# Optimization experiments

Hardware: AMD Instinct MI355X
Metric: run time of the kernel (lower is better)

Reference implementation:

```python
import jax, jax.numpy as jnp
import numpy as np

NUM_STEPS = 3
NUM_HEADS = 8
HEAD_DIM = 128
EPS = 1e-5


def layernorm(x, g, b):
    mu = jnp.mean(x, -1, keepdims=True)
    var = jnp.mean(jnp.square(x - mu), -1, keepdims=True)
    return (x - mu) * jax.lax.rsqrt(var + EPS) * g + b


def entmax15(x):
    # Exact entmax-1.5 along last axis (Peters & Martins 2019, sort-based).
    x = (x - jnp.max(x, -1, keepdims=True)) / 2.0
    xs = jnp.flip(jnp.sort(x, -1), -1)  # descending sort
    rho = jnp.arange(1, x.shape[-1] + 1, dtype=x.dtype)
    mean = jnp.cumsum(xs, -1) / rho
    meansq = jnp.cumsum(xs * xs, -1) / rho
    ss = rho * (meansq - jnp.square(mean))
    tau = mean - jnp.sqrt(jnp.clip((1.0 - ss) / rho, 0.0, None))
    support = jnp.sum(tau <= xs, -1, keepdims=True)
    tau_star = jnp.take_along_axis(tau, support - 1, -1)
    return jnp.square(jnp.clip(x - tau_star, 0.0, None))


def setup_inputs() -> dict:
    key = jax.random.key(0)
    ks = jax.random.split(key, 6)
    B, S, Hd, Md, N = 2, 1024, 2048, 1024, 2048
    THD = NUM_HEADS * HEAD_DIM
    return {
        "hidden": jax.random.normal(ks[0], (B, S, Hd), jnp.float32),
        "memory": jax.random.normal(ks[1], (N, Md), jnp.float32),
        "Wq": jax.random.normal(ks[2], (THD, Hd), jnp.float32) / np.float32(np.sqrt(Hd)),
        "Wk": jax.random.normal(ks[3], (THD, Md), jnp.float32) / np.float32(np.sqrt(Md)),
        "Wv": jax.random.normal(ks[4], (THD, Md), jnp.float32) / np.float32(np.sqrt(Md)),
        "Wo": jax.random.normal(ks[5], (Hd, THD), jnp.float32) / np.float32(np.sqrt(THD)),
        "log_beta": jnp.full((NUM_HEADS,), float(np.log(1.0 / np.sqrt(HEAD_DIM))), jnp.float32),
        "g_state": jnp.ones((Hd,), jnp.float32),
        "b_state": jnp.zeros((Hd,), jnp.float32),
        "g_mem": jnp.ones((Md,), jnp.float32),
        "b_mem": jnp.zeros((Md,), jnp.float32),
    }


def reference(hidden, memory, Wq, Wk, Wv, Wo, log_beta, g_state, b_state, g_mem, b_mem):
    B, S, _ = hidden.shape
    N = memory.shape[0]
    H, hd = NUM_HEADS, HEAD_DIM
    # projections
    Q = layernorm(hidden, g_state, b_state) @ Wq.T            # (B,S,H*hd)
    mn = layernorm(memory, g_mem, b_mem)                      # (N,Md)
    K = (mn @ Wk.T).reshape(N, H, hd).transpose(1, 0, 2)      # (H,N,hd)
    V = (mn @ Wv.T).reshape(N, H, hd).transpose(1, 0, 2)      # (H,N,hd)
    xi = Q.reshape(B, S, H, hd).transpose(0, 2, 1, 3)          # (B,H,S,hd)
    beta = jnp.exp(log_beta)[None, :, None, None]
    for _ in range(NUM_STEPS):
        scores = jnp.einsum('bhsd,hnd->bhsn', xi, K) * beta    # (B,H,S,N)
        w = entmax15(scores)
        xi = jnp.einsum('bhsn,hnd->bhsd', w, V)
    out = xi.transpose(0, 2, 1, 3).reshape(B, S, H * hd) @ Wo.T  # (B,S,hidden_dim)
    return out
```

## Files before the change

kernel.cpp:

```cpp
#include <hip/hip_runtime.h>

typedef _Float16 half8 __attribute__((ext_vector_type(8)));
typedef _Float16 hv4 __attribute__((ext_vector_type(4)));
typedef _Float16 h2 __attribute__((ext_vector_type(2)));
typedef float fv4 __attribute__((ext_vector_type(4)));

typedef __attribute__((address_space(3))) unsigned lds_u32;
typedef const __attribute__((address_space(1))) unsigned glb_u32;

#if defined(__has_builtin)
#if __has_builtin(__builtin_amdgcn_fdot2)
#define FDOT2(a, b, c) __builtin_amdgcn_fdot2((a), (b), (c), false)
#endif
#endif
#ifndef FDOT2
#define FDOT2(a, b, c) ((c) + (float)(a)[0] * (float)(b)[0] + (float)(a)[1] * (float)(b)[1])
#endif

__device__ __forceinline__ h2 pkrtz(float a, float b) {
  return __builtin_bit_cast(h2, __builtin_amdgcn_cvt_pkrtz(a, b));
}

__device__ __forceinline__ void gll16(const void* g, void* l) {
  __builtin_amdgcn_global_load_lds((glb_u32*)g, (lds_u32*)l, 16, 0, 0);
}

__device__ __forceinline__ void ln_body(const float* __restrict__ in, const float* __restrict__ g,
                                        const float* __restrict__ bb, _Float16* __restrict__ out,
                                        int ncols, int row) {
  __shared__ float sm[8];
  int t = threadIdx.x;
  const float* rp = in + (size_t)row * ncols;
  int nv = ncols >> 10;
  fv4 v[2];
  float s1 = 0.f, s2 = 0.f;
#pragma unroll
  for (int c = 0; c < 2; ++c)
    if (c < nv) {
      v[c] = *(const fv4*)(rp + c * 1024 + t * 4);
#pragma unroll
      for (int j = 0; j < 4; ++j) { s1 += v[c][j]; s2 += v[c][j] * v[c][j]; }
    }
#pragma unroll
  for (int off = 32; off > 0; off >>= 1) { s1 += __shfl_xor(s1, off, 64); s2 += __shfl_xor(s2, off, 64); }
  int w = t >> 6;
  if ((t & 63) == 0) { sm[w] = s1; sm[4 + w] = s2; }
  __syncthreads();
  s1 = sm[0] + sm[1] + sm[2] + sm[3];
  s2 = sm[4] + sm[5] + sm[6] + sm[7];
  float inv = 1.0f / (float)ncols;
  float mu = s1 * inv;
  float var = s2 * inv - mu * mu;
  float rstd = rsqrtf(var + 1e-5f);
#pragma unroll
  for (int c = 0; c < 2; ++c)
    if (c < nv) {
      int col = c * 1024 + t * 4;
      fv4 gg = *(const fv4*)(g + col);
      fv4 bv = *(const fv4*)(bb + col);
      hv4 o;
#pragma unroll
      for (int j = 0; j < 4; ++j) o[j] = (_Float16)(((v[c][j] - mu) * rstd) * gg[j] + bv[j]);
      *(hv4*)(out + (size_t)row * ncols + col) = o;
    }
}

__global__ __launch_bounds__(256) void ln_all(const float* __restrict__ hid,
                                              const float* __restrict__ mem,
                                              const float* __restrict__ gs, const float* __restrict__ bs,
                                              const float* __restrict__ gm, const float* __restrict__ bm,
                                              _Float16* __restrict__ oh, _Float16* __restrict__ om) {
  int b = blockIdx.x;
  if (b < 2048) ln_body(hid, gs, bs, oh, 2048, b);
  else ln_body(mem, gm, bm, om, 1024, b - 2048);
}

__global__ __launch_bounds__(256) void cast_all(const float* __restrict__ s0, _Float16* __restrict__ d0,
                                                const float* __restrict__ s1, _Float16* __restrict__ d1,
                                                const float* __restrict__ s2, _Float16* __restrict__ d2,
                                                const float* __restrict__ s3, _Float16* __restrict__ d3) {
  int b = blockIdx.x;
  const float* s;
  _Float16* d;
  int off;
  if (b < 2048) { s = s0; d = d0; off = b; }
  else if (b < 3072) { s = s1; d = d1; off = b - 2048; }
  else if (b < 4096) { s = s2; d = d2; off = b - 3072; }
  else { s = s3; d = d3; off = b - 4096; }
  int i = (off * 256 + threadIdx.x) << 2;
  fv4 f = *(const fv4*)(s + i);
  hv4 h;
#pragma unroll
  for (int j = 0; j < 4; ++j) h[j] = (_Float16)f[j];
  *(hv4*)(d + i) = h;
}

__global__ __launch_bounds__(256) void reduce_split(const float* __restrict__ parts, int ns,
                                                    long long stride,
                                                    _Float16* __restrict__ hi, int n) {
  int i = (blockIdx.x * 256 + threadIdx.x) << 2;
  if (i < n) {
    fv4 s = *(const fv4*)(parts + i);
    for (int j = 1; j < ns; ++j) {
      fv4 v = *(const fv4*)(parts + (size_t)j * stride + i);
      s += v;
    }
    hv4 h;
#pragma unroll
    for (int j = 0; j < 4; ++j) h[j] = (_Float16)s[j];
    *(hv4*)(hi + i) = h;
  }
}

__global__ __launch_bounds__(256, 3) void fused_step(const _Float16* __restrict__ xi,
                                                     const _Float16* __restrict__ kp,
                                                     const _Float16* __restrict__ vt,
                                                     const float* __restrict__ log_beta,
                                                     _Float16* __restrict__ xo) {
  __shared__ __align__(16) _Float16 ring[4 * 3 * 2048];
  __shared__ float red[384];
  float* red4 = (float*)ring;

  int t = threadIdx.x;
  int wv = t >> 6, l = t & 63;
  int lr = l & 15, quad = l >> 4;

  int id = blockIdx.x;
  int h = id & 7;
  int rbb = id >> 3;
  int b = rbb >> 6;
  int r0 = (rbb & 63) << 4;

  const _Float16* xiP = xi + ((size_t)(b * 1024 + r0)) * 1024 + h * 128;
  const _Float16* kP = kp + (size_t)h * 128;
  const _Float16* vP = vt + (size_t)h * 128 * 2048;
  int sbase = wv * 512;

  _Float16* ringW = &ring[wv * 6144];

  float a05 = 0.5f * __expf(log_beta[h]);

  half8 bx[4];
#pragma unroll
  for (int c = 0; c < 4; ++c)
    bx[c] = *(const half8*)(xiP + (size_t)lr * 1024 + c * 32 + quad * 8);
  asm volatile("s_waitcnt vmcnt(0)" ::: "memory");

  int srl = l >> 2;
  int scs = ((l & 3) ^ ((l >> 3) & 3)) << 3;
  int rsw = (lr >> 1) & 3;
  int vsh = ((l & 1) ^ ((l >> 3) & 1)) * 8;
  int hsr = ((quad >> 1) ^ ((lr >> 2) & 1));

  auto stageK = [&](int f) {
    const _Float16* src = kP + (size_t)(sbase + f * 16 + srl) * 1024 + scs;
    _Float16* dst = ringW + (f % 3) * 2048;
#pragma unroll
    for (int g = 0; g < 4; ++g) gll16(src + g * 32, dst + g * 512);
  };
  auto stageV = [&](int f) {
    const _Float16* src = vP + (size_t)(l >> 1) * 2048 + sbase + f * 16 + vsh;
    _Float16* dst = ringW + (f % 3) * 2048;
#pragma unroll
    for (int g = 0; g < 4; ++g) gll16(src + (size_t)g * 32 * 2048, dst + g * 512);
  };

  h2 pk[64];
  float msc = -3.0e38f;
  stageK(0); stageK(1);
#pragma unroll
  for (int f = 0; f < 32; ++f) {
    if (f < 31) asm volatile("s_waitcnt vmcnt(4)" ::: "memory");
    else asm volatile("s_waitcnt vmcnt(0)" ::: "memory");
    __builtin_amdgcn_sched_barrier(0);
    const _Float16* kb = ringW + (f % 3) * 2048;
    half8 ka[4];
#pragma unroll
    for (int g = 0; g < 4; ++g)
      ka[g] = *(const half8*)(kb + g * 512 + lr * 32 + ((quad ^ rsw) << 3));
    if (f + 2 < 32) stageK(f + 2);
    fv4 a = {0.f, 0.f, 0.f, 0.f};
    __builtin_amdgcn_s_setprio(1);
#pragma unroll
    for (int g = 0; g < 4; ++g)
      a = __builtin_amdgcn_mfma_f32_16x16x32_f16(ka[g], bx[g], a, 0, 0, 0);
    __builtin_amdgcn_s_setprio(0);
    msc = fmaxf(fmaxf(msc, fmaxf(a[0], a[1])), fmaxf(a[2], a[3]));
    pk[2 * f] = pkrtz(a05 * a[0], a05 * a[1]);
    pk[2 * f + 1] = pkrtz(a05 * a[2], a05 * a[3]);
  }

  msc = fmaxf(msc, __shfl_xor(msc, 16, 64));
  msc = fmaxf(msc, __shfl_xor(msc, 32, 64));
  if (l < 16) red[wv * 48 + l] = msc;
  __syncthreads();
  msc = fmaxf(fmaxf(red[lr], red[48 + lr]), fmaxf(red[96 + lr], red[144 + lr]));
  float xm = a05 * msc;
  h2 mpk = {(_Float16)xm, (_Float16)xm};
#pragma unroll
  for (int p = 0; p < 64; ++p) pk[p] = pk[p] - mpk;

  h2 one2 = {(_Float16)1.0f, (_Float16)1.0f};
  float tau = -1.0f;
  int par = 1;
#pragma unroll 1
  for (int it = 0; it < 14; ++it) {
    h2 tp = {(_Float16)tau, (_Float16)tau};
    float tq = (float)tp[0];
    float M1 = 0.f, M2 = 0.f;
    unsigned kc = 0;
#pragma unroll
    for (int p = 0; p < 64; ++p) {
      h2 y = __builtin_elementwise_max(pk[p], tp);
      M1 = FDOT2(y, one2, M1);
      M2 = FDOT2(y, y, M2);
      h2 d = tp - y;
      unsigned u = __builtin_bit_cast(unsigned, d);
      kc += (u >> 15) & 0x10001u;
    }
    float kf = (float)((kc & 0xffffu) + (kc >> 16));
    kf += __shfl_xor(kf, 16, 64); kf += __shfl_xor(kf, 32, 64);
    M1 += __shfl_xor(M1, 16, 64); M1 += __shfl_xor(M1, 32, 64);
    M2 += __shfl_xor(M2, 16, 64); M2 += __shfl_xor(M2, 32, 64);
    float* wr = red + par * 192 + wv * 48;
    if (l < 16) { wr[l] = kf; wr[16 + l] = M1; wr[32 + l] = M2; }
    __syncthreads();
    float C = 0.f, S1 = 0.f, S2 = 0.f;
#pragma unroll
    for (int w2 = 0; w2 < 4; ++w2) {
      const float* rr = red + par * 192 + w2 * 48;
      C += rr[lr]; S1 += rr[16 + lr]; S2 += rr[32 + lr];
    }
    par ^= 1;
    S1 = S1 - (2048.0f - C) * tq;
    S2 = S2 - (2048.0f - C) * tq * tq;
    float mean = S1 / C;
    float ssv = S2 - S1 * mean;
    float nt = mean - sqrtf(fmaxf((1.0f - ssv) / C, 0.0f));
    bool conv = fabsf(nt - tau) < 1e-4f;
    tau = nt;
    if (__all(conv)) break;
  }

  {
    h2 tp = {(_Float16)tau, (_Float16)tau};
#pragma unroll
    for (int p = 0; p < 64; ++p) {
      h2 y = __builtin_elementwise_max(pk[p], tp);
      h2 d = y - tp;
      pk[p] = d * d;
    }
  }

  fv4 acc[8] = {};
  stageV(0); stageV(1);
#pragma unroll
  for (int f = 0; f < 32; ++f) {
    if (f < 31) asm volatile("s_waitcnt vmcnt(4)" ::: "memory");
    else asm volatile("s_waitcnt vmcnt(0)" ::: "memory");
    __builtin_amdgcn_sched_barrier(0);
    const _Float16* vb = ringW + (f % 3) * 2048;
    hv4 bv[8];
#pragma unroll
    for (int ni = 0; ni < 8; ++ni)
      bv[ni] = *(const hv4*)(vb + (ni >> 1) * 512 + ((ni & 1) * 16 + lr) * 16 + hsr * 8 + (quad & 1) * 4);
    if (f + 2 < 32) stageV(f + 2);
    hv4 aw4 = {pk[2 * f][0], pk[2 * f][1], pk[2 * f + 1][0], pk[2 * f + 1][1]};
    __builtin_amdgcn_s_setprio(1);
#pragma unroll
    for (int ni = 0; ni < 8; ++ni)
      acc[ni] = __builtin_amdgcn_mfma_f32_16x16x16f16(aw4, bv[ni], acc[ni], 0, 0, 0);
    __builtin_amdgcn_s_setprio(0);
  }

  __syncthreads();
#pragma unroll
  for (int ni = 0; ni < 8; ++ni)
#pragma unroll
    for (int r = 0; r < 4; ++r)
      red4[wv * 2048 + (quad * 4 + r) * 128 + ni * 16 + lr] = acc[ni][r];
  __syncthreads();
#pragma unroll
  for (int g = 0; g < 2; ++g) {
    int idx = wv * 512 + g * 256 + l * 4;
    fv4 s = *(const fv4*)&red4[idx];
    s += *(const fv4*)&red4[idx + 2048];
    s += *(const fv4*)&red4[idx + 4096];
    s += *(const fv4*)&red4[idx + 6144];
    int row = idx >> 7, dim = idx & 127;
    hv4 o;
#pragma unroll
    for (int j = 0; j < 4; ++j) o[j] = (_Float16)s[j];
    *(hv4*)(xo + ((size_t)(b * 1024 + r0 + row)) * 1024 + h * 128 + dim) = o;
  }
}

struct GemmParams {
  const _Float16 *A, *B, *B2;
  _Float16 *C16, *C16b;
  float* C32;
  int K, lda, ldb;
  long long aSB, aSH, bSH;
  long long cSB, cSH, cOsR, cOsC;
  long long cOsRb, cOsCb;
  long long partStride;
  int outMode, outModeB, nsplit, dual;
  int gx, gy, swz;
};

__device__ __forceinline__ void gemm_body(const GemmParams& p, int bx, int by, int bz) {
  __shared__ __align__(16) _Float16 As[3][128 * 32];
  __shared__ __align__(16) _Float16 Bs[3][128 * 32];
  int t = threadIdx.x;
  int m0 = by * 128;
  int n0, kbeg, kend, ks = 0;
  if (p.nsplit > 1) {
    ks = bx % p.nsplit;
    n0 = (bx / p.nsplit) * 128;
    int kl = p.K / p.nsplit;
    kbeg = ks * kl;
    kend = kbeg + kl;
  } else {
    n0 = bx * 128;
    kbeg = 0;
    kend = p.K;
  }
  int bidx, h, job = 0;
  if (p.dual) { job = bz; bidx = 0; h = 0; }
  else { bidx = bz >> 3; h = bz & 7; }
  const _Float16* pA = p.A + bidx * p.aSB + h * p.aSH;
  const _Float16* pB = (job ? p.B2 : p.B) + h * p.bSH;

  fv4 acc[4][4] = {};
  int wv = t >> 6, l = t & 63, quad = l >> 4, lr = l & 15;
  int wm = (wv >> 1) * 64, wn = (wv & 1) * 64;
  int rl = l >> 2;
  int cs = (((l & 3) ^ ((l >> 3) & 3)) << 3);
  int rsw = (lr >> 1) & 3;

  auto STAGE = [&](int buf, int k0) {
#pragma unroll
    for (int v = 0; v < 2; ++v) {
      int rb = wv * 16 + v * 64;
      int r = rb + rl;
      gll16(pA + (size_t)(m0 + r) * p.lda + k0 + cs, &As[buf][rb * 32]);
      gll16(pB + (size_t)(n0 + r) * p.ldb + k0 + cs, &Bs[buf][rb * 32]);
    }
  };

  int nk = (kend - kbeg) >> 5;
  STAGE(0, kbeg);
  if (nk > 1) STAGE(1, kbeg + 32);
  int cur = 0;
  for (int ti = 0; ti < nk; ++ti) {
    if (ti + 1 < nk) asm volatile("s_waitcnt vmcnt(4)" ::: "memory");
    else asm volatile("s_waitcnt vmcnt(0)" ::: "memory");
    __builtin_amdgcn_s_barrier();
    __builtin_amdgcn_sched_barrier(0);
    if (ti + 2 < nk) {
      int nb = cur + 2;
      if (nb >= 3) nb -= 3;
      STAGE(nb, kbeg + ((ti + 2) << 5));
    }
    __builtin_amdgcn_sched_barrier(0);
    half8 ah[4], bh[4];
#pragma unroll
    for (int mi = 0; mi < 4; ++mi)
      ah[mi] = *(const half8*)&As[cur][(wm + mi * 16 + lr) * 32 + ((quad ^ rsw) << 3)];
#pragma unroll
    for (int ni = 0; ni < 4; ++ni)
      bh[ni] = *(const half8*)&Bs[cur][(wn + ni * 16 + lr) * 32 + ((quad ^ rsw) << 3)];
    __builtin_amdgcn_s_setprio(1);
#pragma unroll
    for (int mi = 0; mi < 4; ++mi)
#pragma unroll
      for (int ni = 0; ni < 4; ++ni)
        acc[mi][ni] = __builtin_amdgcn_mfma_f32_16x16x32_f16(ah[mi], bh[ni], acc[mi][ni], 0, 0, 0);
    __builtin_amdgcn_s_setprio(0);
    cur = (cur == 2) ? 0 : cur + 1;
  }

  int om = (p.dual && job) ? p.outModeB : p.outMode;
  _Float16* c16 = (p.dual && job) ? p.C16b : p.C16;
  long long osR = (p.dual && job) ? p.cOsRb : p.cOsR;
  long long osC = (p.dual && job) ? p.cOsCb : p.cOsC;
  float* c32 = p.C32 + (p.nsplit > 1 ? (long long)ks * p.partStride : 0);
  long long cOff = (long long)bidx * p.cSB + (long long)h * p.cSH;
#pragma unroll
  for (int mi = 0; mi < 4; ++mi)
#pragma unroll
    for (int ni = 0; ni < 4; ++ni) {
      int row = m0 + wm + mi * 16 + quad * 4;
      int col = n0 + wn + ni * 16 + lr;
#pragma unroll
      for (int r = 0; r < 4; ++r) {
        float val = acc[mi][ni][r];
        long long idx = cOff + (long long)(row + r) * osR + (long long)col * osC;
        if (om == 1) c32[idx] = val;
        else c16[idx] = (_Float16)val;
      }
    }
}

__global__ __launch_bounds__(256) void gemm_nt(GemmParams p) {
  int id = blockIdx.x;
  if (p.swz) {
    int q = (int)gridDim.x >> 3;
    id = (id & 7) * q + (id >> 3);
  }
  int bx = id % p.gx;
  int r = id / p.gx;
  gemm_body(p, bx, r % p.gy, r / p.gy);
}

__global__ __launch_bounds__(256) void gemm_pair(GemmParams a, GemmParams b, int na) {
  int id = blockIdx.x;
  if (id < na) {
    int bx = id % a.gx;
    int r = id / a.gx;
    gemm_body(a, bx, r % a.gy, r / a.gy);
  } else {
    int j = id - na;
    int bx = j % b.gx;
    int r = j / b.gx;
    gemm_body(b, bx, r % b.gy, r / b.gy);
  }
}

extern "C" void kernel_launch(void* const* d_in, const int* in_sizes, int n_in,
                              void* d_out, int out_size, void* d_ws, size_t ws_size,
                              hipStream_t stream) {
  const float* hidden = (const float*)d_in[0];
  const float* memory = (const float*)d_in[1];
  const float* Wq = (const float*)d_in[2];
  const float* Wk = (const float*)d_in[3];
  const float* Wv = (const float*)d_in[4];
  const float* Wo = (const float*)d_in[5];
  const float* log_beta = (const float*)d_in[6];
  const float* g_state = (const float*)d_in[7];
  const float* b_state = (const float*)d_in[8];
  const float* g_mem = (const float*)d_in[9];
  const float* b_mem = (const float*)d_in[10];

  char* w = (char*)d_ws;
  auto alloc = [&](size_t bytes) {
    char* r = w;
    w += (bytes + 255) & ~(size_t)255;
    return r;
  };
  _Float16* wq16 = (_Float16*)alloc(2097152 * 2);
  _Float16* wk16 = (_Float16*)alloc(1048576 * 2);
  _Float16* wv16 = (_Float16*)alloc(1048576 * 2);
  _Float16* wo16 = (_Float16*)alloc(2097152 * 2);
  _Float16* lnh16 = (_Float16*)alloc(4194304 * 2);
  _Float16* mn16 = (_Float16*)alloc(2097152 * 2);
  _Float16* kph = (_Float16*)alloc(2097152 * 2);
  _Float16* vt16 = (_Float16*)alloc(2097152 * 2);
  _Float16* xih = (_Float16*)alloc(2097152 * 2);
  float* parts = (float*)alloc((size_t)2 * 2097152 * 4);

  ln_all<<<4096, 256, 0, stream>>>(hidden, memory, g_state, b_state, g_mem, b_mem, lnh16, mn16);
  cast_all<<<6144, 256, 0, stream>>>(Wq, wq16, Wk, wk16, Wv, wv16, Wo, wo16);

  {
    GemmParams pq{};
    pq.A = lnh16; pq.lda = 2048;
    pq.B = wq16; pq.ldb = 2048;
    pq.K = 2048; pq.nsplit = 2;
    pq.C32 = parts; pq.outMode = 1; pq.partStride = 2097152;
    pq.cOsR = 1024; pq.cOsC = 1;
    pq.gx = 16; pq.gy = 16;

    GemmParams pkv{};
    pkv.A = mn16; pkv.lda = 1024;
    pkv.B = wk16; pkv.B2 = wv16; pkv.ldb = 1024;
    pkv.K = 1024; pkv.dual = 1;
    pkv.C16 = kph; pkv.outMode = 0; pkv.cOsR = 1024; pkv.cOsC = 1;
    pkv.C16b = vt16; pkv.outModeB = 0; pkv.cOsRb = 1; pkv.cOsCb = 2048;
    pkv.gx = 8; pkv.gy = 16;

    gemm_pair<<<512, 256, 0, stream>>>(pq, pkv, 256);
    reduce_split<<<2048, 256, 0, stream>>>(parts, 2, 2097152, xih, 2097152);
  }

  for (int step = 0; step < 3; ++step)
    fused_step<<<1024, 256, 0, stream>>>(xih, kph, vt16, log_beta, xih);

  {
    GemmParams p{};
    p.A = xih; p.lda = 1024;
    p.B = wo16; p.ldb = 1024;
    p.K = 1024;
    p.C32 = (float*)d_out; p.outMode = 1;
    p.cOsR = 2048; p.cOsC = 1;
    p.gx = 16; p.gy = 16; p.swz = 1;
    gemm_nt<<<256, 256, 0, stream>>>(p);
  }
}
```

Baseline: 489.4 us.

## Process 32 query rows per block in fused_step to reuse K/V tiles

Result: slower. 516.8 us (+5.6%).

```diff
diff --git a/kernel.cpp b/kernel.cpp
--- a/kernel.cpp
+++ b/kernel.cpp
@@ -23,6 +23,11 @@
 
 __device__ __forceinline__ void gll16(const void* g, void* l) {
   __builtin_amdgcn_global_load_lds((glb_u32*)g, (lds_u32*)l, 16, 0, 0);
+}
+
+__device__ __forceinline__ void barrier_lds() {
+  asm volatile("s_waitcnt lgkmcnt(0)" ::: "memory");
+  __builtin_amdgcn_s_barrier();
 }
 
 __device__ __forceinline__ void ln_body(const float* __restrict__ in, const float* __restrict__ g,
@@ -112,13 +117,13 @@
   }
 }
 
-__global__ __launch_bounds__(256, 3) void fused_step(const _Float16* __restrict__ xi,
+__global__ __launch_bounds__(256, 2) void fused_step(const _Float16* __restrict__ xi,
                                                      const _Float16* __restrict__ kp,
                                                      const _Float16* __restrict__ vt,
                                                      const float* __restrict__ log_beta,
                                                      _Float16* __restrict__ xo) {
   __shared__ __align__(16) _Float16 ring[4 * 3 * 2048];
-  __shared__ float red[384];
+  __shared__ float red[768];
   float* red4 = (float*)ring;
 
   int t = threadIdx.x;
@@ -128,8 +133,8 @@
   int id = blockIdx.x;
   int h = id & 7;
   int rbb = id >> 3;
-  int b = rbb >> 6;
-  int r0 = (rbb & 63) << 4;
+  int b = rbb >> 5;
+  int r0 = (rbb & 31) << 5;
 
   const _Float16* xiP = xi + ((size_t)(b * 1024 + r0)) * 1024 + h * 128;
   const _Float16* kP = kp + (size_t)h * 128;
@@ -140,10 +145,12 @@
 
   float a05 = 0.5f * __expf(log_beta[h]);
 
-  half8 bx[4];
-#pragma unroll
-  for (int c = 0; c < 4; ++c)
+  half8 bx[4], bx2[4];
+#pragma unroll
+  for (int c = 0; c < 4; ++c) {
     bx[c] = *(const half8*)(xiP + (size_t)lr * 1024 + c * 32 + quad * 8);
+    bx2[c] = *(const half8*)(xiP + (size_t)(16 + lr) * 1024 + c * 32 + quad * 8);
+  }
   asm volatile("s_waitcnt vmcnt(0)" ::: "memory");
 
   int srl = l >> 2;
@@ -165,8 +172,8 @@
     for (int g = 0; g < 4; ++g) gll16(src + (size_t)g * 32 * 2048, dst + g * 512);
   };
 
-  h2 pk[64];
-  float msc = -3.0e38f;
+  h2 pk[64], pk2[64];
+  float msc = -3.0e38f, msc2 = -3.0e38f;
   stageK(0); stageK(1);
 #pragma unroll
   for (int f = 0; f < 32; ++f) {
@@ -180,80 +187,113 @@
       ka[g] = *(const half8*)(kb + g * 512 + lr * 32 + ((quad ^ rsw) << 3));
     if (f + 2 < 32) stageK(f + 2);
     fv4 a = {0.f, 0.f, 0.f, 0.f};
+    fv4 a2 = {0.f, 0.f, 0.f, 0.f};
     __builtin_amdgcn_s_setprio(1);
 #pragma unroll
-    for (int g = 0; g < 4; ++g)
+    for (int g = 0; g < 4; ++g) {
       a = __builtin_amdgcn_mfma_f32_16x16x32_f16(ka[g], bx[g], a, 0, 0, 0);
+      a2 = __builtin_amdgcn_mfma_f32_16x16x32_f16(ka[g], bx2[g], a2, 0, 0, 0);
+    }
     __builtin_amdgcn_s_setprio(0);
     msc = fmaxf(fmaxf(msc, fmaxf(a[0], a[1])), fmaxf(a[2], a[3]));
+    msc2 = fmaxf(fmaxf(msc2, fmaxf(a2[0], a2[1])), fmaxf(a2[2], a2[3]));
     pk[2 * f] = pkrtz(a05 * a[0], a05 * a[1]);
     pk[2 * f + 1] = pkrtz(a05 * a[2], a05 * a[3]);
-  }
+    pk2[2 * f] = pkrtz(a05 * a2[0], a05 * a2[1]);
+    pk2[2 * f + 1] = pkrtz(a05 * a2[2], a05 * a2[3]);
+  }
+
+  asm volatile("s_waitcnt lgkmcnt(0)" ::: "memory");
+  __builtin_amdgcn_sched_barrier(0);
+  stageV(0); stageV(1);
 
   msc = fmaxf(msc, __shfl_xor(msc, 16, 64));
   msc = fmaxf(msc, __shfl_xor(msc, 32, 64));
-  if (l < 16) red[wv * 48 + l] = msc;
-  __syncthreads();
-  msc = fmaxf(fmaxf(red[lr], red[48 + lr]), fmaxf(red[96 + lr], red[144 + lr]));
-  float xm = a05 * msc;
-  h2 mpk = {(_Float16)xm, (_Float16)xm};
-#pragma unroll
-  for (int p = 0; p < 64; ++p) pk[p] = pk[p] - mpk;
+  msc2 = fmaxf(msc2, __shfl_xor(msc2, 16, 64));
+  msc2 = fmaxf(msc2, __shfl_xor(msc2, 32, 64));
+  if (l < 16) { red[wv * 16 + l] = msc; red[64 + wv * 16 + l] = msc2; }
+  barrier_lds();
+  float m = fmaxf(fmaxf(red[lr], red[16 + lr]), fmaxf(red[32 + lr], red[48 + lr]));
+  float m2 = fmaxf(fmaxf(red[64 + lr], red[80 + lr]), fmaxf(red[96 + lr], red[112 + lr]));
+  {
+    float xm = a05 * m, xm2 = a05 * m2;
+    h2 mpk = {(_Float16)xm, (_Float16)xm};
+    h2 mpk2 = {(_Float16)xm2, (_Float16)xm2};
+#pragma unroll
+    for (int p = 0; p < 64; ++p) { pk[p] = pk[p] - mpk; pk2[p] = pk2[p] - mpk2; }
+  }
 
   h2 one2 = {(_Float16)1.0f, (_Float16)1.0f};
-  float tau = -1.0f;
+  float tau = -1.0f, tau2 = -1.0f;
   int par = 1;
 #pragma unroll 1
   for (int it = 0; it < 14; ++it) {
     h2 tp = {(_Float16)tau, (_Float16)tau};
-    float tq = (float)tp[0];
-    float M1 = 0.f, M2 = 0.f;
-    unsigned kc = 0;
+    h2 tp2 = {(_Float16)tau2, (_Float16)tau2};
+    float tq = (float)tp[0], tq2 = (float)tp2[0];
+    float M1 = 0.f, M2 = 0.f, N1 = 0.f, N2 = 0.f;
+    unsigned kc = 0, kc2 = 0;
 #pragma unroll
     for (int p = 0; p < 64; ++p) {
       h2 y = __builtin_elementwise_max(pk[p], tp);
       M1 = FDOT2(y, one2, M1);
       M2 = FDOT2(y, y, M2);
-      h2 d = tp - y;
-      unsigned u = __builtin_bit_cast(unsigned, d);
+      unsigned u = __builtin_bit_cast(unsigned, h2(tp - y));
       kc += (u >> 15) & 0x10001u;
+      h2 y2 = __builtin_elementwise_max(pk2[p], tp2);
+      N1 = FDOT2(y2, one2, N1);
+      N2 = FDOT2(y2, y2, N2);
+      unsigned u2 = __builtin_bit_cast(unsigned, h2(tp2 - y2));
+      kc2 += (u2 >> 15) & 0x10001u;
     }
     float kf = (float)((kc & 0xffffu) + (kc >> 16));
+    float kf2 = (float)((kc2 & 0xffffu) + (kc2 >> 16));
     kf += __shfl_xor(kf, 16, 64); kf += __shfl_xor(kf, 32, 64);
     M1 += __shfl_xor(M1, 16, 64); M1 += __shfl_xor(M1, 32, 64);
     M2 += __shfl_xor(M2, 16, 64); M2 += __shfl_xor(M2, 32, 64);
-    float* wr = red + par * 192 + wv * 48;
-    if (l < 16) { wr[l] = kf; wr[16 + l] = M1; wr[32 + l] = M2; }
-    __syncthreads();
-    float C = 0.f, S1 = 0.f, S2 = 0.f;
+    kf2 += __shfl_xor(kf2, 16, 64); kf2 += __shfl_xor(kf2, 32, 64);
+    N1 += __shfl_xor(N1, 16, 64); N1 += __shfl_xor(N1, 32, 64);
+    N2 += __shfl_xor(N2, 16, 64); N2 += __shfl_xor(N2, 32, 64);
+    float* wr = red + par * 384 + wv * 96;
+    if (l < 16) {
+      wr[l] = kf; wr[16 + l] = M1; wr[32 + l] = M2;
+      wr[48 + l] = kf2; wr[64 + l] = N1; wr[80 + l] = N2;
+    }
+    barrier_lds();
+    float C = 0.f, S1 = 0.f, S2 = 0.f, C2 = 0.f, T1 = 0.f, T2 = 0.f;
 #pragma unroll
     for (int w2 = 0; w2 < 4; ++w2) {
-      const float* rr = red + par * 192 + w2 * 48;
+      const float* rr = red + par * 384 + w2 * 96;
       C += rr[lr]; S1 += rr[16 + lr]; S2 += rr[32 + lr];
+      C2 += rr[48 + lr]; T1 += rr[64 + lr]; T2 += rr[80 + lr];
     }
     par ^= 1;
     S1 = S1 - (2048.0f - C) * tq;
     S2 = S2 - (2048.0f - C) * tq * tq;
+    T1 = T1 - (2048.0f - C2) * tq2;
+    T2 = T2 - (2048.0f - C2) * tq2 * tq2;
     float mean = S1 / C;
-    float ssv = S2 - S1 * mean;
-    float nt = mean - sqrtf(fmaxf((1.0f - ssv) / C, 0.0f));
-    bool conv = fabsf(nt - tau) < 1e-4f;
-    tau = nt;
+    float nt = mean - sqrtf(fmaxf((1.0f - (S2 - S1 * mean)) / C, 0.0f));
+    float mean2 = T1 / C2;
+    float nt2 = mean2 - sqrtf(fmaxf((1.0f - (T2 - T1 * mean2)) / C2, 0.0f));
+    bool conv = (fabsf(nt - tau) < 1e-4f) && (fabsf(nt2 - tau2) < 1e-4f);
+    tau = nt; tau2 = nt2;
     if (__all(conv)) break;
   }
 
   {
     h2 tp = {(_Float16)tau, (_Float16)tau};
+    h2 tp2 = {(_Float16)tau2, (_Float16)tau2};
 #pragma unroll
     for (int p = 0; p < 64; ++p) {
-      h2 y = __builtin_elementwise_max(pk[p], tp);
-      h2 d = y - tp;
-      pk[p] = d * d;
-    }
-  }
-
-  fv4 acc[8] = {};
-  stageV(0); stageV(1);
+      h2 y = __builtin_elementwise_max(pk[p], tp) - tp;
+      pk[p] = y * y;
+      h2 y2 = __builtin_elementwise_max(pk2[p], tp2) - tp2;
+      pk2[p] = y2 * y2;
+    }
+  }
+
+  fv4 acc[8] = {}, ac2[8] = {};
 #pragma unroll
   for (int f = 0; f < 32; ++f) {
     if (f < 31) asm volatile("s_waitcnt vmcnt(4)" ::: "memory");
@@ -266,32 +306,37 @@
       bv[ni] = *(const hv4*)(vb + (ni >> 1) * 512 + ((ni & 1) * 16 + lr) * 16 + hsr * 8 + (quad & 1) * 4);
     if (f + 2 < 32) stageV(f + 2);
     hv4 aw4 = {pk[2 * f][0], pk[2 * f][1], pk[2 * f + 1][0], pk[2 * f + 1][1]};
+    hv4 aw4b = {pk2[2 * f][0], pk2[2 * f][1], pk2[2 * f + 1][0], pk2[2 * f + 1][1]};
     __builtin_amdgcn_s_setprio(1);
 #pragma unroll
+    for (int ni = 0; ni < 8; ++ni) {
+      acc[ni] = __builtin_amdgcn_mfma_f32_16x16x16f16(aw4, bv[ni], acc[ni], 0, 0, 0);
+      ac2[ni] = __builtin_amdgcn_mfma_f32_16x16x16f16(aw4b, bv[ni], ac2[ni], 0, 0, 0);
+    }
+    __builtin_amdgcn_s_setprio(0);
+  }
+
+#pragma unroll
+  for (int grp = 0; grp < 2; ++grp) {
+    __syncthreads();
+#pragma unroll
     for (int ni = 0; ni < 8; ++ni)
-      acc[ni] = __builtin_amdgcn_mfma_f32_16x16x16f16(aw4, bv[ni], acc[ni], 0, 0, 0);
-    __builtin_amdgcn_s_setprio(0);
-  }
-
-  __syncthreads();
-#pragma unroll
-  for (int ni = 0; ni < 8; ++ni)
-#pragma unroll
-    for (int r = 0; r < 4; ++r)
-      red4[wv * 2048 + (quad * 4 + r) * 128 + ni * 16 + lr] = acc[ni][r];
-  __syncthreads();
-#pragma unroll
-  for (int g = 0; g < 2; ++g) {
-    int idx = wv * 512 + g * 256 + l * 4;
-    fv4 s = *(const fv4*)&red4[idx];
-    s += *(const fv4*)&red4[idx + 2048];
-    s += *(const fv4*)&red4[idx + 4096];
-    s += *(const fv4*)&red4[idx + 6144];
-    int row = idx >> 7, dim = idx & 127;
-    hv4 o;
-#pragma unroll
-    for (int j = 0; j < 4; ++j) o[j] = (_Float16)s[j];
-    *(hv4*)(xo + ((size_t)(b * 1024 + r0 + row)) * 1024 + h * 128 + dim) = o;
+#pragma unroll
+      for (int r = 0; r < 4; ++r)
+        red4[wv * 2112 + (quad * 4 + r) * 132 + ni * 16 + lr] = (grp ? ac2 : acc)[ni][r];
+    __syncthreads();
+    int row = t >> 4, c = t & 15;
+    fv4 sA = {0.f, 0.f, 0.f, 0.f}, sB = {0.f, 0.f, 0.f, 0.f};
+#pragma unroll
+    for (int w2 = 0; w2 < 4; ++w2) {
+      const float* rr = red4 + w2 * 2112 + row * 132 + c * 8;
+      sA += *(const fv4*)rr;
+      sB += *(const fv4*)(rr + 4);
+    }
+    half8 o;
+#pragma unroll
+    for (int j = 0; j < 4; ++j) { o[j] = (_Float16)sA[j]; o[4 + j] = (_Float16)sB[j]; }
+    *(half8*)(xo + ((size_t)(b * 1024 + r0 + grp * 16 + row)) * 1024 + h * 128 + c * 8) = o;
   }
 }
 
@@ -484,7 +529,7 @@
   }
 
   for (int step = 0; step < 3; ++step)
-    fused_step<<<1024, 256, 0, stream>>>(xih, kph, vt16, log_beta, xih);
+    fused_step<<<512, 256, 0, stream>>>(xih, kph, vt16, log_beta, xih);
 
   {
     GemmParams p{};
```

## Shrink fused_step LDS ring to double buffer for higher occupancy

Applied to the files above, without the earlier changes.

Result: slower. 532.6 us (+8.8%).

```diff
diff --git a/kernel.cpp b/kernel.cpp
--- a/kernel.cpp
+++ b/kernel.cpp
@@ -23,6 +23,11 @@
 
 __device__ __forceinline__ void gll16(const void* g, void* l) {
   __builtin_amdgcn_global_load_lds((glb_u32*)g, (lds_u32*)l, 16, 0, 0);
+}
+
+__device__ __forceinline__ void barrier_lds() {
+  asm volatile("s_waitcnt lgkmcnt(0)" ::: "memory");
+  __builtin_amdgcn_s_barrier();
 }
 
 __device__ __forceinline__ void ln_body(const float* __restrict__ in, const float* __restrict__ g,
@@ -112,12 +117,12 @@
   }
 }
 
-__global__ __launch_bounds__(256, 3) void fused_step(const _Float16* __restrict__ xi,
+__global__ __launch_bounds__(256, 4) void fused_step(const _Float16* __restrict__ xi,
                                                      const _Float16* __restrict__ kp,
                                                      const _Float16* __restrict__ vt,
                                                      const float* __restrict__ log_beta,
                                                      _Float16* __restrict__ xo) {
-  __shared__ __align__(16) _Float16 ring[4 * 3 * 2048];
+  __shared__ __align__(16) _Float16 ring[4 * 2 * 2048];
   __shared__ float red[384];
   float* red4 = (float*)ring;
 
@@ -136,7 +141,7 @@
   const _Float16* vP = vt + (size_t)h * 128 * 2048;
   int sbase = wv * 512;
 
-  _Float16* ringW = &ring[wv * 6144];
+  _Float16* ringW = &ring[wv * 4096];
 
   float a05 = 0.5f * __expf(log_beta[h]);
 
@@ -154,13 +159,13 @@
 
   auto stageK = [&](int f) {
     const _Float16* src = kP + (size_t)(sbase + f * 16 + srl) * 1024 + scs;
-    _Float16* dst = ringW + (f % 3) * 2048;
+    _Float16* dst = ringW + (f & 1) * 2048;
 #pragma unroll
     for (int g = 0; g < 4; ++g) gll16(src + g * 32, dst + g * 512);
   };
   auto stageV = [&](int f) {
     const _Float16* src = vP + (size_t)(l >> 1) * 2048 + sbase + f * 16 + vsh;
-    _Float16* dst = ringW + (f % 3) * 2048;
+    _Float16* dst = ringW + (f & 1) * 2048;
 #pragma unroll
     for (int g = 0; g < 4; ++g) gll16(src + (size_t)g * 32 * 2048, dst + g * 512);
   };
@@ -173,28 +178,32 @@
     if (f < 31) asm volatile("s_waitcnt vmcnt(4)" ::: "memory");
     else asm volatile("s_waitcnt vmcnt(0)" ::: "memory");
     __builtin_amdgcn_sched_barrier(0);
-    const _Float16* kb = ringW + (f % 3) * 2048;
+    const _Float16* kb = ringW + (f & 1) * 2048;
     half8 ka[4];
 #pragma unroll
     for (int g = 0; g < 4; ++g)
       ka[g] = *(const half8*)(kb + g * 512 + lr * 32 + ((quad ^ rsw) << 3));
-    if (f + 2 < 32) stageK(f + 2);
     fv4 a = {0.f, 0.f, 0.f, 0.f};
     __builtin_amdgcn_s_setprio(1);
 #pragma unroll
     for (int g = 0; g < 4; ++g)
       a = __builtin_amdgcn_mfma_f32_16x16x32_f16(ka[g], bx[g], a, 0, 0, 0);
     __builtin_amdgcn_s_setprio(0);
+    __builtin_amdgcn_sched_barrier(0);
+    if (f + 2 < 32) stageK(f + 2);
     msc = fmaxf(fmaxf(msc, fmaxf(a[0], a[1])), fmaxf(a[2], a[3]));
     pk[2 * f] = pkrtz(a05 * a[0], a05 * a[1]);
     pk[2 * f + 1] = pkrtz(a05 * a[2], a05 * a[3]);
   }
 
+  __builtin_amdgcn_sched_barrier(0);
+  stageV(0); stageV(1);
+
   msc = fmaxf(msc, __shfl_xor(msc, 16, 64));
   msc = fmaxf(msc, __shfl_xor(msc, 32, 64));
-  if (l < 16) red[wv * 48 + l] = msc;
-  __syncthreads();
-  msc = fmaxf(fmaxf(red[lr], red[48 + lr]), fmaxf(red[96 + lr], red[144 + lr]));
+  if (l < 16) red[wv * 16 + l] = msc;
+  barrier_lds();
+  msc = fmaxf(fmaxf(red[lr], red[16 + lr]), fmaxf(red[32 + lr], red[48 + lr]));
   float xm = a05 * msc;
   h2 mpk = {(_Float16)xm, (_Float16)xm};
 #pragma unroll
@@ -214,8 +223,7 @@
       h2 y = __builtin_elementwise_max(pk[p], tp);
       M1 = FDOT2(y, one2, M1);
       M2 = FDOT2(y, y, M2);
-      h2 d = tp - y;
-      unsigned u = __builtin_bit_cast(unsigned, d);
+      unsigned u = __builtin_bit_cast(unsigned, h2(tp - y));
       kc += (u >> 15) & 0x10001u;
     }
     float kf = (float)((kc & 0xffffu) + (kc >> 16));
@@ -224,7 +232,7 @@
     M2 += __shfl_xor(M2, 16, 64); M2 += __shfl_xor(M2, 32, 64);
     float* wr = red + par * 192 + wv * 48;
     if (l < 16) { wr[l] = kf; wr[16 + l] = M1; wr[32 + l] = M2; }
-    __syncthreads();
+    barrier_lds();
     float C = 0.f, S1 = 0.f, S2 = 0.f;
 #pragma unroll
     for (int w2 = 0; w2 < 4; ++w2) {
@@ -246,31 +254,30 @@
     h2 tp = {(_Float16)tau, (_Float16)tau};
 #pragma unroll
     for (int p = 0; p < 64; ++p) {
-      h2 y = __builtin_elementwise_max(pk[p], tp);
-      h2 d = y - tp;
-      pk[p] = d * d;
+      h2 y = __builtin_elementwise_max(pk[p], tp) - tp;
+      pk[p] = y * y;
     }
   }
 
   fv4 acc[8] = {};
-  stageV(0); stageV(1);
 #pragma unroll
   for (int f = 0; f < 32; ++f) {
     if (f < 31) asm volatile("s_waitcnt vmcnt(4)" ::: "memory");
     else asm volatile("s_waitcnt vmcnt(0)" ::: "memory");
     __builtin_amdgcn_sched_barrier(0);
-    const _Float16* vb = ringW + (f % 3) * 2048;
+    const _Float16* vb = ringW + (f & 1) * 2048;
     hv4 bv[8];
 #pragma unroll
     for (int ni = 0; ni < 8; ++ni)
       bv[ni] = *(const hv4*)(vb + (ni >> 1) * 512 + ((ni & 1) * 16 + lr) * 16 + hsr * 8 + (quad & 1) * 4);
-    if (f + 2 < 32) stageV(f + 2);
     hv4 aw4 = {pk[2 * f][0], pk[2 * f][1], pk[2 * f + 1][0], pk[2 * f + 1][1]};
     __builtin_amdgcn_s_setprio(1);
 #pragma unroll
     for (int ni = 0; ni < 8; ++ni)
       acc[ni] = __builtin_amdgcn_mfma_f32_16x16x16f16(aw4, bv[ni], acc[ni], 0, 0, 0);
     __builtin_amdgcn_s_setprio(0);
+    __builtin_amdgcn_sched_barrier(0);
+    if (f + 2 < 32) stageV(f + 2);
   }
 
   __syncthreads();
@@ -278,20 +285,22 @@
   for (int ni = 0; ni < 8; ++ni)
 #pragma unroll
     for (int r = 0; r < 4; ++r)
-      red4[wv * 2048 + (quad * 4 + r) * 128 + ni * 16 + lr] = acc[ni][r];
+      red4[wv * 2048 + (quad * 4 + r) * 128 + ((ni * 16 + lr) ^ (quad << 4))] = acc[ni][r];
   __syncthreads();
-#pragma unroll
-  for (int g = 0; g < 2; ++g) {
-    int idx = wv * 512 + g * 256 + l * 4;
-    fv4 s = *(const fv4*)&red4[idx];
-    s += *(const fv4*)&red4[idx + 2048];
-    s += *(const fv4*)&red4[idx + 4096];
-    s += *(const fv4*)&red4[idx + 6144];
-    int row = idx >> 7, dim = idx & 127;
-    hv4 o;
-#pragma unroll
-    for (int j = 0; j < 4; ++j) o[j] = (_Float16)s[j];
-    *(hv4*)(xo + ((size_t)(b * 1024 + r0 + row)) * 1024 + h * 128 + dim) = o;
+  {
+    int row = t >> 4, c = t & 15;
+    int pc = (c * 8) ^ ((row >> 2) << 4);
+    fv4 sA = {0.f, 0.f, 0.f, 0.f}, sB = {0.f, 0.f, 0.f, 0.f};
+#pragma unroll
+    for (int w2 = 0; w2 < 4; ++w2) {
+      const float* rr = red4 + w2 * 2048 + row * 128 + pc;
+      sA += *(const fv4*)rr;
+      sB += *(const fv4*)(rr + 4);
+    }
+    half8 o;
+#pragma unroll
+    for (int j = 0; j < 4; ++j) { o[j] = (_Float16)sA[j]; o[4 + j] = (_Float16)sB[j]; }
+    *(half8*)(xo + ((size_t)(b * 1024 + r0 + row)) * 1024 + h * 128 + c * 8) = o;
   }
 }
 
```
